# Optimization experiments

Hardware: AMD Instinct MI355X
Metric: run time of the kernel (lower is better)

## Reference

```python
import jax, jax.numpy as jnp
import numpy as np
import math

ALPHA = 0.25
GAMMA = 2.0
IMG = 640.0


def setup_inputs() -> dict:
    key = jax.random.key(0)
    k0, k1, k2, k3, k4, k5, k6, k7 = jax.random.split(key, 8)
    B, A, C, N = 8, 250000, 4, 16
    classifications = jax.random.uniform(k0, (B, A, C), minval=0.01, maxval=0.99, dtype=jnp.float32)
    regressions = jax.random.normal(k1, (B, A, 4), dtype=jnp.float32) * 0.1
    # anchors as (x1, y1, x2, y2) with x1<x2, y1<y2
    ctr = jax.random.uniform(k2, (A, 2), minval=0.0, maxval=IMG, dtype=jnp.float32)
    half = jax.random.uniform(k3, (A, 2), minval=2.0, maxval=32.0, dtype=jnp.float32)
    anchors_pos = jnp.concatenate([ctr - half, ctr + half], axis=1)
    # annotations: (cx, cy, angle, length, class); all valid (class != -1)
    ann_xy = jax.random.uniform(k4, (B, N, 2), minval=50.0, maxval=IMG - 50.0, dtype=jnp.float32)
    ann_th = jax.random.uniform(k5, (B, N, 1), minval=-math.pi / 2, maxval=math.pi / 2, dtype=jnp.float32)
    ann_len = jax.random.uniform(k6, (B, N, 1), minval=10.0, maxval=100.0, dtype=jnp.float32)
    ann_cls = jax.random.randint(k7, (B, N, 1), 0, C).astype(jnp.float32)
    annotations = jnp.concatenate([ann_xy, ann_th, ann_len, ann_cls], axis=2)
    return {"classifications": classifications, "regressions": regressions,
            "anchors_pos": anchors_pos, "annotations": annotations}


def coordinates_transform(anchors_pos):
    x1, y1, x2, y2 = anchors_pos[:, 0], anchors_pos[:, 1], anchors_pos[:, 2], anchors_pos[:, 3]
    ctr_x = (x1 + x2) / 2
    ctr_y = (y1 + y2) / 2
    width = x2 - x1
    height = y2 - y1
    length = jnp.sqrt((x2 - x1) ** 2 + (y2 - y1) ** 2)
    vert = x1 == x2
    safe_dx = jnp.where(vert, 1.0, x2 - x1)
    theta = jnp.where(vert, jnp.sign(y2 - y1) * (math.pi / 2), jnp.arctan((y2 - y1) / safe_dx))
    return ctr_x, ctr_y, width, height, length, theta


def calc_iou(anchors_pos, cal_annotations):
    # anchors_pos [A,4], cal_annotations [N,4] -> IoU [A,N]
    centers = cal_annotations[:, :2]
    ang = cal_annotations[:, 2]
    lng = cal_annotations[:, 3]
    dx = jnp.abs(0.5 * lng * jnp.cos(ang))[:, None]
    dy = jnp.abs(0.5 * lng * jnp.sin(ang))[:, None]
    lt = centers - jnp.concatenate([dx, dy], axis=1)
    rb = centers + jnp.concatenate([dx, dy], axis=1)
    bbox = jnp.concatenate([lt, rb], axis=1)  # [N,4]
    area = (bbox[:, 2] - bbox[:, 0]) * (bbox[:, 3] - bbox[:, 1])  # [N]
    iw = jnp.minimum(anchors_pos[:, 2][:, None], bbox[:, 2]) - jnp.maximum(anchors_pos[:, 0][:, None], bbox[:, 0])
    ih = jnp.minimum(anchors_pos[:, 3][:, None], bbox[:, 3]) - jnp.maximum(anchors_pos[:, 1][:, None], bbox[:, 1])
    iw = jnp.maximum(iw, 0.0)
    ih = jnp.maximum(ih, 0.0)
    a_area = ((anchors_pos[:, 2] - anchors_pos[:, 0]) * (anchors_pos[:, 3] - anchors_pos[:, 1]))[:, None]
    ua = jnp.maximum(a_area + area - iw * ih, 1e-8)
    return (iw * ih) / ua


def smooth_l1_rows(pred, gt):
    # per-row mean smooth-L1 over the 4 (cx, cy, theta, length) components
    d = pred - gt
    ad = jnp.abs(d)
    return jnp.mean(jnp.where(ad < 1.0, 0.5 * d * d, ad - 0.5), axis=-1)


def _per_image(classification, regression, annotation, anchors_pos, geom):
    A = anchors_pos.shape[0]
    C = classification.shape[1]
    cls = jnp.clip(classification, 1e-4, 1.0 - 1e-4)
    valid = annotation[:, 4] != -1.0  # [N]
    IoU = calc_iou(anchors_pos, annotation[:, :4])  # [A,N]
    IoU = jnp.where(valid[None, :], IoU, -1.0)
    IoU_max = IoU.max(axis=1)
    IoU_argmax = IoU.argmax(axis=1)
    pos = IoU_max >= 0.5
    neg = IoU_max < 0.4
    # targets: -1 ignore, 0 background, 1 assigned class
    targets = jnp.where((pos | neg)[:, None], 0.0, -1.0)  # [A,C]
    assigned = annotation[IoU_argmax]  # [A,5]
    onehot = jax.nn.one_hot(assigned[:, 4].astype(jnp.int32), C, dtype=jnp.float32)
    targets = jnp.where(pos[:, None] * onehot == 1.0, 1.0, targets)
    # force-assign best anchor for any annotation whose max IoU < 0.5
    ann_max = IoU.max(axis=0)     # [N]
    ann_arg = IoU.argmax(axis=0)  # [N]
    force = valid & (ann_max < 0.5)
    idx = jnp.where(force, ann_arg, A)  # A = out-of-bounds -> dropped
    ann_cls_idx = annotation[:, 4].astype(jnp.int32)
    targets = targets.at[idx].set(0.0, mode='drop')
    targets = targets.at[idx, ann_cls_idx].set(1.0, mode='drop')
    assigned = assigned.at[idx].set(annotation, mode='drop')
    positive = targets.sum(axis=-1) > 0.0  # [A]
    num_pos = positive.sum().astype(jnp.float32)
    # focal loss
    bce = -(targets * jnp.log(cls) + (1.0 - targets) * jnp.log(1.0 - cls))
    p_t = jnp.where(targets == 1.0, cls, 1.0 - cls)
    fl = (1.0 - p_t) ** GAMMA * bce
    alpha_f = jnp.where(targets == 1.0, ALPHA, 1.0 - ALPHA)
    fl = jnp.where(targets != -1.0, alpha_f * fl, 0.0)
    cls_loss = fl.sum() / jnp.maximum(num_pos, 1.0)
    ctr_x, ctr_y, w, h, L, th = geom
    pred_cx = regression[:, 0] * w + ctr_x
    pred_cy = regression[:, 1] * h + ctr_y
    pred_th = regression[:, 2] + th
    pred_len = jnp.exp(regression[:, 3]) * L
    pred_cal = jnp.stack([pred_cx, pred_cy, pred_th, pred_len], axis=1)  # [A,4]
    per_anchor = smooth_l1_rows(pred_cal, assigned[:, :4])
    reg_loss = jnp.sum(jnp.where(positive, per_anchor, 0.0)) / jnp.maximum(num_pos, 1.0)
    return cls_loss, reg_loss


def reference(classifications, regressions, anchors_pos, annotations):
    geom = coordinates_transform(anchors_pos)
    cls_l, reg_l = jax.vmap(lambda c, r, a: _per_image(c, r, a, anchors_pos, geom))(
        classifications, regressions, annotations)
    return (jnp.mean(cls_l, keepdims=True), jnp.mean(reg_l, keepdims=True))
```

## Files before the change

kernel.cpp:

```cpp
#include <hip/hip_runtime.h>
#include <math.h>

#define A_TOTAL 250000
#define BCNT 8
#define NANN 16
#define GX 128
#define NTHR 256
#define STRIDE (GX * NTHR)
#define IDXM 0x3FFFFu
#define QMASK 0xFFFC0000u


__device__ __forceinline__ float rfl(float x) {
    return __uint_as_float(__builtin_amdgcn_readfirstlane(__float_as_uint(x)));
}

__device__ __forceinline__ float4 pred_cal(float4 ap, float4 r, float aw, float ah) {
    float cxa = (ap.x + ap.z) * 0.5f, cya = (ap.y + ap.w) * 0.5f;
    float L = sqrtf(aw * aw + ah * ah);
    float th = (ap.x == ap.z) ? copysignf(1.5707963267948966f, ah) : atanf(ah / aw);
    return make_float4(r.x * aw + cxa, r.y * ah + cya, r.z + th, expf(r.w) * L);
}

__device__ __forceinline__ float sl1(float4 pr, float4 g) {
    float s = 0.f, d, ad;
    d = pr.x - g.x; ad = fabsf(d); s += (ad < 1.f) ? 0.5f * d * d : ad - 0.5f;
    d = pr.y - g.y; ad = fabsf(d); s += (ad < 1.f) ? 0.5f * d * d : ad - 0.5f;
    d = pr.z - g.z; ad = fabsf(d); s += (ad < 1.f) ? 0.5f * d * d : ad - 0.5f;
    d = pr.w - g.w; ad = fabsf(d); s += (ad < 1.f) ? 0.5f * d * d : ad - 0.5f;
    return s * 0.25f;
}

__device__ __forceinline__ float focal4m(float4 p4, unsigned mask) {
    float pv[4] = {p4.x, p4.y, p4.z, p4.w};
    float fl = 0.f;
#pragma unroll
    for (int c = 0; c < 4; c++) {
        float pc = fminf(fmaxf(pv[c], 1e-4f), 1.f - 1e-4f);
        fl += ((mask >> c) & 1) ? 0.25f * (1.f - pc) * (1.f - pc) * (-__logf(pc))
                                : 0.75f * pc * pc * (-__logf(1.f - pc));
    }
    return fl;
}

__global__ __launch_bounds__(256) void detloss_init(
    const float* __restrict__ ann, float* __restrict__ table)
{
    int tid = threadIdx.x;
    if (tid < BCNT * NANN) {
        int b = tid >> 4, n = tid & 15;
        const float* a5 = ann + tid * 5;
        float cx = a5[0], cy = a5[1], th = a5[2], ln = a5[3], cl = a5[4];
        bool valid = (cl != -1.0f);
        float dx = fabsf(0.5f * ln * cosf(th));
        float dy = fabsf(0.5f * ln * sinf(th));
        float x1 = cx - dx, y1 = cy - dy, x2 = cx + dx, y2 = cy + dy;
        float ar = (x2 - x1) * (y2 - y1);
        if (!valid) { x1 = y1 = x2 = y2 = 3.0e8f; ar = 1.0e30f; }
        float* tb = table + b * 160;
        tb[4 * n + 0] = x1; tb[4 * n + 1] = y1; tb[4 * n + 2] = x2; tb[4 * n + 3] = y2;
        tb[64 + n] = ar;
        tb[80 + 4 * n + 0] = cx; tb[80 + 4 * n + 1] = cy;
        tb[80 + 4 * n + 2] = th; tb[80 + 4 * n + 3] = ln;
        tb[144 + n] = cl;
    }
}

__global__ __launch_bounds__(NTHR, 4) void detloss_main(
    const float* __restrict__ cls, const float* __restrict__ reg,
    const float* __restrict__ anchors, const float* __restrict__ table,
    unsigned* __restrict__ part)
{
    int b = blockIdx.y;
    int tid = threadIdx.x;
    __shared__ float sGT[NANN][5];
    __shared__ unsigned sKey[4][NANN];
    __shared__ float sPart[4][3];

    const float* tb = table + b * 160;
    if (tid < NANN) {
        sGT[tid][0] = tb[80 + 4 * tid + 0]; sGT[tid][1] = tb[80 + 4 * tid + 1];
        sGT[tid][2] = tb[80 + 4 * tid + 2]; sGT[tid][3] = tb[80 + 4 * tid + 3];
        sGT[tid][4] = tb[144 + tid];
    }

    float sx1[NANN], sy1[NANN], sx2[NANN], sy2[NANN], bar[NANN];
#pragma unroll
    for (int n = 0; n < NANN; n++) {
        sx1[n] = rfl(tb[4 * n + 0]); sy1[n] = rfl(tb[4 * n + 1]);
        sx2[n] = rfl(tb[4 * n + 2]); sy2[n] = rfl(tb[4 * n + 3]);
        bar[n] = rfl(tb[64 + n]);
    }
    __syncthreads();

    unsigned bmk[NANN];
#pragma unroll
    for (int n = 0; n < NANN; n++) bmk[n] = 0u;
    float clsS = 0.f, regS = 0.f, nposS = 0.f;

    const float4* clsB = (const float4*)(cls + (size_t)b * A_TOTAL * 4);
    const float4* regB = (const float4*)(reg + (size_t)b * A_TOTAL * 4);
    const float4* anc4 = (const float4*)anchors;

    int a = blockIdx.x * NTHR + tid;
    float4 ap = anc4[a];
    while (a < A_TOTAL) {
        float4 p4 = clsB[a];
        int a2 = a + STRIDE;
        int apre = (a2 < A_TOTAL) ? a2 : a;
        float4 apn = anc4[apre];
        unsigned inv_a = IDXM - (unsigned)a;

        float aw = ap.z - ap.x, ah = ap.w - ap.y;
        float aarea = aw * ah;
        float best = 0.f; int barg = 0;
#pragma unroll
        for (int n = 0; n < NANN; n++) {
            float iw = fminf(ap.z, sx2[n]) - fmaxf(ap.x, sx1[n]);
            float ih = fminf(ap.w, sy2[n]) - fmaxf(ap.y, sy1[n]);
            iw = fmaxf(iw, 0.f); ih = fmaxf(ih, 0.f);
            float inter = iw * ih;
            float ua = fmaxf(aarea + bar[n] - inter, 1e-8f);
            float iou = inter * __builtin_amdgcn_rcpf(ua);
            if (iou > best) { best = iou; barg = n; }
            unsigned kc = (__float_as_uint(iou) & QMASK) | inv_a;
            bmk[n] = (kc > bmk[n]) ? kc : bmk[n];
        }
        if (best < 0.4f || best >= 0.5f) {
            bool pos = (best >= 0.5f);
            float pc0 = fminf(fmaxf(p4.x, 1e-4f), 1.f - 1e-4f);
            float pc1 = fminf(fmaxf(p4.y, 1e-4f), 1.f - 1e-4f);
            float pc2 = fminf(fmaxf(p4.z, 1e-4f), 1.f - 1e-4f);
            float pc3 = fminf(fmaxf(p4.w, 1e-4f), 1.f - 1e-4f);
            float fl = 0.75f * pc0 * pc0 * (-__logf(1.f - pc0))
                     + 0.75f * pc1 * pc1 * (-__logf(1.f - pc1))
                     + 0.75f * pc2 * pc2 * (-__logf(1.f - pc2))
                     + 0.75f * pc3 * pc3 * (-__logf(1.f - pc3));
            if (pos) {
                int ac = (int)sGT[barg][4];
                float pc = ac == 0 ? pc0 : ac == 1 ? pc1 : ac == 2 ? pc2 : pc3;
                fl += 0.25f * (1.f - pc) * (1.f - pc) * (-__logf(pc))
                    - 0.75f * pc * pc * (-__logf(1.f - pc));
                nposS += 1.f;
                float4 r = regB[a];
                float4 pr = pred_cal(ap, r, aw, ah);
                float4 g = make_float4(sGT[barg][0], sGT[barg][1], sGT[barg][2], sGT[barg][3]);
                regS += sl1(pr, g);
            }
            clsS += fl;
        }
        ap = apn; a = a2;
    }

    int lane = tid & 63, wv = tid >> 6;
#pragma unroll
    for (int n = 0; n < NANN; n++) {
        unsigned k = bmk[n];
#pragma unroll
        for (int off = 1; off < 64; off <<= 1) {
            unsigned o = __shfl_xor(k, off, 64);
            k = (o > k) ? o : k;
        }
        if (lane == 0) sKey[wv][n] = k;
    }
#pragma unroll
    for (int off = 1; off < 64; off <<= 1) {
        clsS  += __shfl_xor(clsS, off, 64);
        regS  += __shfl_xor(regS, off, 64);
        nposS += __shfl_xor(nposS, off, 64);
    }
    if (lane == 0) { sPart[wv][0] = clsS; sPart[wv][1] = regS; sPart[wv][2] = nposS; }
    __syncthreads();

    unsigned* pb = part + ((size_t)(b * GX + blockIdx.x)) * 32;
    if (tid < NANN) {
        unsigned m = sKey[0][tid];
#pragma unroll
        for (int w = 1; w < 4; w++) m = (sKey[w][tid] > m) ? sKey[w][tid] : m;
        pb[tid] = m;
    }
    if (tid == 0) {
        float c0 = 0, c1 = 0, c2 = 0;
        for (int w = 0; w < 4; w++) { c0 += sPart[w][0]; c1 += sPart[w][1]; c2 += sPart[w][2]; }
        ((float*)pb)[16] = c0;
        ((float*)pb)[17] = c1;
        ((float*)pb)[18] = c2;
    }
}

__global__ __launch_bounds__(256) void detloss_reduce(
    const float* __restrict__ cls, const float* __restrict__ reg,
    const float* __restrict__ anchors, const float* __restrict__ table,
    const unsigned* __restrict__ part, float* __restrict__ out)
{
    int tid = threadIdx.x;
    __shared__ unsigned rKey[BCNT][NANN];
    __shared__ float rAcc[BCNT][3];
    __shared__ int fForce[BCNT * NANN];
    __shared__ float fAcc[BCNT * 3];

    if (tid < BCNT * NANN) {
        int b = tid >> 4, n = tid & 15;
        unsigned m = 0u;
        for (int k = 0; k < GX; k++) {
            unsigned v = part[((size_t)(b * GX + k)) * 32 + n];
            m = (v > m) ? v : m;
        }
        rKey[b][n] = m;
    } else if (tid < BCNT * NANN + BCNT * 3) {
        int t = tid - BCNT * NANN; int b = t / 3, j = t % 3;
        float s = 0.f;
        for (int k = 0; k < GX; k++)
            s += ((const float*)part)[((size_t)(b * GX + k)) * 32 + 16 + j];
        rAcc[b][j] = s;
    }
    if (tid < BCNT * 3) fAcc[tid] = 0.f;
    __syncthreads();

    if (tid < BCNT * NANN) {
        int b = tid >> 4, n = tid & 15;
        unsigned k = rKey[b][n];
        float amax = __uint_as_float(k & QMASK);
        float cl = table[b * 160 + 144 + n];
        bool force = (cl != -1.f) && (amax < 0.5f);
        int anchor = (int)(IDXM - (k & IDXM));
        fForce[tid] = (force && anchor >= 0 && anchor < A_TOTAL) ? anchor : -1;
    }
    __syncthreads();

    if (tid < BCNT * NANN) {
        int fb = tid >> 4, fn = tid & 15;
        const float* tbf = table + fb * 160;
        int idx = fForce[tid];
        bool first = (idx >= 0);
        for (int m = 0; m < fn; m++) if (fForce[fb * NANN + m] == idx) first = false;
        if (idx >= 0 && first) {
            const float4* clsBf = (const float4*)(cls + (size_t)fb * A_TOTAL * 4);
            const float4* regBf = (const float4*)(reg + (size_t)fb * A_TOTAL * 4);
            float4 ap2 = ((const float4*)anchors)[idx];
            float aw = ap2.z - ap2.x, ah = ap2.w - ap2.y;
            float aarea = aw * ah;
            float best = 0.f; int barg = 0;
#pragma unroll
            for (int m = 0; m < NANN; m++) {
                float iw = fminf(ap2.z, tbf[4 * m + 2]) - fmaxf(ap2.x, tbf[4 * m + 0]);
                float ih = fminf(ap2.w, tbf[4 * m + 3]) - fmaxf(ap2.y, tbf[4 * m + 1]);
                iw = fmaxf(iw, 0.f); ih = fmaxf(ih, 0.f);
                float inter = iw * ih;
                float ua = fmaxf(aarea + tbf[64 + m] - inter, 1e-8f);
                float iou = inter * __builtin_amdgcn_rcpf(ua);
                if (iou > best) { best = iou; barg = m; }
            }
            float4 p4 = clsBf[idx];
            float oldc = 0.f, oldr = 0.f, oldn = 0.f;
            if (best < 0.4f || best >= 0.5f) {
                bool pos = (best >= 0.5f);
                unsigned msk = pos ? (1u << (int)tbf[144 + barg]) : 0u;
                oldc = focal4m(p4, msk);
                if (pos) {
                    oldn = 1.f;
                    float4 r = regBf[idx];
                    float4 pr = pred_cal(ap2, r, aw, ah);
                    float4 g = make_float4(tbf[80 + 4 * barg + 0], tbf[80 + 4 * barg + 1],
                                           tbf[80 + 4 * barg + 2], tbf[80 + 4 * barg + 3]);
                    oldr = sl1(pr, g);
                }
            }
            unsigned cmask = 0; int lastm = fn;
            for (int m = 0; m < NANN; m++)
                if (fForce[fb * NANN + m] == idx) { cmask |= 1u << (int)tbf[144 + m]; lastm = m; }
            float newc = focal4m(p4, cmask);
            float4 r = regBf[idx];
            float4 pr = pred_cal(ap2, r, aw, ah);
            float4 g = make_float4(tbf[80 + 4 * lastm + 0], tbf[80 + 4 * lastm + 1],
                                   tbf[80 + 4 * lastm + 2], tbf[80 + 4 * lastm + 3]);
            float newr = sl1(pr, g);
            atomicAdd(&fAcc[fb * 3 + 0], newc - oldc);
            atomicAdd(&fAcc[fb * 3 + 1], newr - oldr);
            atomicAdd(&fAcc[fb * 3 + 2], 1.f - oldn);
        }
    }
    __syncthreads();
    if (tid == 0) {
        float cm = 0.f, rm = 0.f;
        for (int b = 0; b < BCNT; b++) {
            float np = fmaxf(rAcc[b][2] + fAcc[b * 3 + 2], 1.f);
            cm += (rAcc[b][0] + fAcc[b * 3 + 0]) / np;
            rm += (rAcc[b][1] + fAcc[b * 3 + 1]) / np;
        }
        out[0] = cm * 0.125f;
        out[1] = rm * 0.125f;
    }
}

extern "C" void kernel_launch(void* const* d_in, const int* in_sizes, int n_in,
                              void* d_out, int out_size, void* d_ws, size_t ws_size,
                              hipStream_t stream) {
    const float* classifications = (const float*)d_in[0];
    const float* regressions     = (const float*)d_in[1];
    const float* anchors_pos     = (const float*)d_in[2];
    const float* annotations     = (const float*)d_in[3];
    float* out = (float*)d_out;

    char* ws = (char*)d_ws;
    float* table = (float*)(ws + 0);
    unsigned* part = (unsigned*)(ws + 8192);

    detloss_init<<<1, 256, 0, stream>>>(annotations, table);
    detloss_main<<<dim3(GX, BCNT), NTHR, 0, stream>>>(
        classifications, regressions, anchors_pos, table, part);
    detloss_reduce<<<1, 256, 0, stream>>>(
        classifications, regressions, anchors_pos, table, part, out);
}
```

Before: 51.30 us.

## Fold annotation table setup into main and reduce kernels, defer argmax recompute

Removes the separate init kernel launch: each main block now computes its annotation box bounds and areas inline from the raw annotations, and the reduce kernel builds its own shared-memory table. The hot IoU loop tracks only the max IoU with fmaxf, and the argmax index is recomputed by a second IoU pass only for positive anchors. This saves one launch and a dependent kernel boundary plus some per-anchor select instructions. In exchange every block redundantly evaluates sin/cos for 16 annotations, and positive anchors pay a second IoU loop.

```diff
diff --git a/kernel.cpp b/kernel.cpp
--- a/kernel.cpp
+++ b/kernel.cpp
@@ -43,32 +43,21 @@
     return fl;
 }
 
-__global__ __launch_bounds__(256) void detloss_init(
-    const float* __restrict__ ann, float* __restrict__ table)
+__device__ __forceinline__ void ann_consts(const float* a5,
+    float& x1, float& y1, float& x2, float& y2, float& ar)
 {
-    int tid = threadIdx.x;
-    if (tid < BCNT * NANN) {
-        int b = tid >> 4, n = tid & 15;
-        const float* a5 = ann + tid * 5;
-        float cx = a5[0], cy = a5[1], th = a5[2], ln = a5[3], cl = a5[4];
-        bool valid = (cl != -1.0f);
-        float dx = fabsf(0.5f * ln * cosf(th));
-        float dy = fabsf(0.5f * ln * sinf(th));
-        float x1 = cx - dx, y1 = cy - dy, x2 = cx + dx, y2 = cy + dy;
-        float ar = (x2 - x1) * (y2 - y1);
-        if (!valid) { x1 = y1 = x2 = y2 = 3.0e8f; ar = 1.0e30f; }
-        float* tb = table + b * 160;
-        tb[4 * n + 0] = x1; tb[4 * n + 1] = y1; tb[4 * n + 2] = x2; tb[4 * n + 3] = y2;
-        tb[64 + n] = ar;
-        tb[80 + 4 * n + 0] = cx; tb[80 + 4 * n + 1] = cy;
-        tb[80 + 4 * n + 2] = th; tb[80 + 4 * n + 3] = ln;
-        tb[144 + n] = cl;
-    }
+    float cx = a5[0], cy = a5[1], th = a5[2], ln = a5[3], cl = a5[4];
+    bool valid = (cl != -1.0f);
+    float dx = fabsf(0.5f * ln * cosf(th));
+    float dy = fabsf(0.5f * ln * sinf(th));
+    x1 = cx - dx; y1 = cy - dy; x2 = cx + dx; y2 = cy + dy;
+    ar = (x2 - x1) * (y2 - y1);
+    if (!valid) { x1 = y1 = x2 = y2 = 3.0e8f; ar = 1.0e30f; }
 }
 
 __global__ __launch_bounds__(NTHR, 4) void detloss_main(
     const float* __restrict__ cls, const float* __restrict__ reg,
-    const float* __restrict__ anchors, const float* __restrict__ table,
+    const float* __restrict__ anchors, const float* __restrict__ ann,
     unsigned* __restrict__ part)
 {
     int b = blockIdx.y;
@@ -77,19 +66,20 @@
     __shared__ unsigned sKey[4][NANN];
     __shared__ float sPart[4][3];
 
-    const float* tb = table + b * 160;
     if (tid < NANN) {
-        sGT[tid][0] = tb[80 + 4 * tid + 0]; sGT[tid][1] = tb[80 + 4 * tid + 1];
-        sGT[tid][2] = tb[80 + 4 * tid + 2]; sGT[tid][3] = tb[80 + 4 * tid + 3];
-        sGT[tid][4] = tb[144 + tid];
+        const float* a5 = ann + (b * NANN + tid) * 5;
+        sGT[tid][0] = a5[0]; sGT[tid][1] = a5[1]; sGT[tid][2] = a5[2];
+        sGT[tid][3] = a5[3]; sGT[tid][4] = a5[4];
     }
 
     float sx1[NANN], sy1[NANN], sx2[NANN], sy2[NANN], bar[NANN];
 #pragma unroll
     for (int n = 0; n < NANN; n++) {
-        sx1[n] = rfl(tb[4 * n + 0]); sy1[n] = rfl(tb[4 * n + 1]);
-        sx2[n] = rfl(tb[4 * n + 2]); sy2[n] = rfl(tb[4 * n + 3]);
-        bar[n] = rfl(tb[64 + n]);
+        const float* a5 = ann + (b * NANN + n) * 5;
+        float x1, y1, x2, y2, ar;
+        ann_consts(a5, x1, y1, x2, y2, ar);
+        sx1[n] = rfl(x1); sy1[n] = rfl(y1); sx2[n] = rfl(x2); sy2[n] = rfl(y2);
+        bar[n] = rfl(ar);
     }
     __syncthreads();
 
@@ -113,7 +103,7 @@
 
         float aw = ap.z - ap.x, ah = ap.w - ap.y;
         float aarea = aw * ah;
-        float best = 0.f; int barg = 0;
+        float best = 0.f;
 #pragma unroll
         for (int n = 0; n < NANN; n++) {
             float iw = fminf(ap.z, sx2[n]) - fmaxf(ap.x, sx1[n]);
@@ -122,7 +112,7 @@
             float inter = iw * ih;
             float ua = fmaxf(aarea + bar[n] - inter, 1e-8f);
             float iou = inter * __builtin_amdgcn_rcpf(ua);
-            if (iou > best) { best = iou; barg = n; }
+            best = fmaxf(best, iou);
             unsigned kc = (__float_as_uint(iou) & QMASK) | inv_a;
             bmk[n] = (kc > bmk[n]) ? kc : bmk[n];
         }
@@ -137,6 +127,17 @@
                      + 0.75f * pc2 * pc2 * (-__logf(1.f - pc2))
                      + 0.75f * pc3 * pc3 * (-__logf(1.f - pc3));
             if (pos) {
+                int barg = 0;
+#pragma unroll
+                for (int n = NANN - 1; n >= 0; n--) {
+                    float iw = fminf(ap.z, sx2[n]) - fmaxf(ap.x, sx1[n]);
+                    float ih = fminf(ap.w, sy2[n]) - fmaxf(ap.y, sy1[n]);
+                    iw = fmaxf(iw, 0.f); ih = fmaxf(ih, 0.f);
+                    float inter = iw * ih;
+                    float ua = fmaxf(aarea + bar[n] - inter, 1e-8f);
+                    float iou = inter * __builtin_amdgcn_rcpf(ua);
+                    if (iou == best) barg = n;
+                }
                 int ac = (int)sGT[barg][4];
                 float pc = ac == 0 ? pc0 : ac == 1 ? pc1 : ac == 2 ? pc2 : pc3;
                 fl += 0.25f * (1.f - pc) * (1.f - pc) * (-__logf(pc))
@@ -190,14 +191,25 @@
 
 __global__ __launch_bounds__(256) void detloss_reduce(
     const float* __restrict__ cls, const float* __restrict__ reg,
-    const float* __restrict__ anchors, const float* __restrict__ table,
+    const float* __restrict__ anchors, const float* __restrict__ ann,
     const unsigned* __restrict__ part, float* __restrict__ out)
 {
     int tid = threadIdx.x;
+    __shared__ float fTab[BCNT * NANN][10];
     __shared__ unsigned rKey[BCNT][NANN];
     __shared__ float rAcc[BCNT][3];
     __shared__ int fForce[BCNT * NANN];
     __shared__ float fAcc[BCNT * 3];
+
+    if (tid < BCNT * NANN) {
+        const float* a5 = ann + tid * 5;
+        float x1, y1, x2, y2, ar;
+        ann_consts(a5, x1, y1, x2, y2, ar);
+        fTab[tid][0] = x1; fTab[tid][1] = y1; fTab[tid][2] = x2; fTab[tid][3] = y2;
+        fTab[tid][4] = ar;
+        fTab[tid][5] = a5[0]; fTab[tid][6] = a5[1]; fTab[tid][7] = a5[2];
+        fTab[tid][8] = a5[3]; fTab[tid][9] = a5[4];
+    }
 
     if (tid < BCNT * NANN) {
         int b = tid >> 4, n = tid & 15;
@@ -221,7 +233,7 @@
         int b = tid >> 4, n = tid & 15;
         unsigned k = rKey[b][n];
         float amax = __uint_as_float(k & QMASK);
-        float cl = table[b * 160 + 144 + n];
+        float cl = fTab[b * NANN + n][9];
         bool force = (cl != -1.f) && (amax < 0.5f);
         int anchor = (int)(IDXM - (k & IDXM));
         fForce[tid] = (force && anchor >= 0 && anchor < A_TOTAL) ? anchor : -1;
@@ -230,7 +242,6 @@
 
     if (tid < BCNT * NANN) {
         int fb = tid >> 4, fn = tid & 15;
-        const float* tbf = table + fb * 160;
         int idx = fForce[tid];
         bool first = (idx >= 0);
         for (int m = 0; m < fn; m++) if (fForce[fb * NANN + m] == idx) first = false;
@@ -240,41 +251,54 @@
             float4 ap2 = ((const float4*)anchors)[idx];
             float aw = ap2.z - ap2.x, ah = ap2.w - ap2.y;
             float aarea = aw * ah;
-            float best = 0.f; int barg = 0;
+            float best = 0.f;
 #pragma unroll
             for (int m = 0; m < NANN; m++) {
-                float iw = fminf(ap2.z, tbf[4 * m + 2]) - fmaxf(ap2.x, tbf[4 * m + 0]);
-                float ih = fminf(ap2.w, tbf[4 * m + 3]) - fmaxf(ap2.y, tbf[4 * m + 1]);
+                const float* t = fTab[fb * NANN + m];
+                float iw = fminf(ap2.z, t[2]) - fmaxf(ap2.x, t[0]);
+                float ih = fminf(ap2.w, t[3]) - fmaxf(ap2.y, t[1]);
                 iw = fmaxf(iw, 0.f); ih = fmaxf(ih, 0.f);
                 float inter = iw * ih;
-                float ua = fmaxf(aarea + tbf[64 + m] - inter, 1e-8f);
+                float ua = fmaxf(aarea + t[4] - inter, 1e-8f);
                 float iou = inter * __builtin_amdgcn_rcpf(ua);
-                if (iou > best) { best = iou; barg = m; }
+                best = fmaxf(best, iou);
+            }
+            int barg = 0;
+#pragma unroll
+            for (int m = NANN - 1; m >= 0; m--) {
+                const float* t = fTab[fb * NANN + m];
+                float iw = fminf(ap2.z, t[2]) - fmaxf(ap2.x, t[0]);
+                float ih = fminf(ap2.w, t[3]) - fmaxf(ap2.y, t[1]);
+                iw = fmaxf(iw, 0.f); ih = fmaxf(ih, 0.f);
+                float inter = iw * ih;
+                float ua = fmaxf(aarea + t[4] - inter, 1e-8f);
+                float iou = inter * __builtin_amdgcn_rcpf(ua);
+                if (iou == best) barg = m;
             }
             float4 p4 = clsBf[idx];
             float oldc = 0.f, oldr = 0.f, oldn = 0.f;
             if (best < 0.4f || best >= 0.5f) {
                 bool pos = (best >= 0.5f);
-                unsigned msk = pos ? (1u << (int)tbf[144 + barg]) : 0u;
+                unsigned msk = pos ? (1u << (int)fTab[fb * NANN + barg][9]) : 0u;
                 oldc = focal4m(p4, msk);
                 if (pos) {
                     oldn = 1.f;
                     float4 r = regBf[idx];
                     float4 pr = pred_cal(ap2, r, aw, ah);
-                    float4 g = make_float4(tbf[80 + 4 * barg + 0], tbf[80 + 4 * barg + 1],
-                                           tbf[80 + 4 * barg + 2], tbf[80 + 4 * barg + 3]);
-                    oldr = sl1(pr, g);
+                    const float* t = fTab[fb * NANN + barg];
+                    oldr = sl1(pr, make_float4(t[5], t[6], t[7], t[8]));
                 }
             }
             unsigned cmask = 0; int lastm = fn;
             for (int m = 0; m < NANN; m++)
-                if (fForce[fb * NANN + m] == idx) { cmask |= 1u << (int)tbf[144 + m]; lastm = m; }
+                if (fForce[fb * NANN + m] == idx) {
+                    cmask |= 1u << (int)fTab[fb * NANN + m][9]; lastm = m;
+                }
             float newc = focal4m(p4, cmask);
             float4 r = regBf[idx];
             float4 pr = pred_cal(ap2, r, aw, ah);
-            float4 g = make_float4(tbf[80 + 4 * lastm + 0], tbf[80 + 4 * lastm + 1],
-                                   tbf[80 + 4 * lastm + 2], tbf[80 + 4 * lastm + 3]);
-            float newr = sl1(pr, g);
+            const float* t = fTab[fb * NANN + lastm];
+            float newr = sl1(pr, make_float4(t[5], t[6], t[7], t[8]));
             atomicAdd(&fAcc[fb * 3 + 0], newc - oldc);
             atomicAdd(&fAcc[fb * 3 + 1], newr - oldr);
             atomicAdd(&fAcc[fb * 3 + 2], 1.f - oldn);
@@ -302,13 +326,10 @@
     const float* annotations     = (const float*)d_in[3];
     float* out = (float*)d_out;
 
-    char* ws = (char*)d_ws;
-    float* table = (float*)(ws + 0);
-    unsigned* part = (unsigned*)(ws + 8192);
-
-    detloss_init<<<1, 256, 0, stream>>>(annotations, table);
+    unsigned* part = (unsigned*)d_ws;
+
     detloss_main<<<dim3(GX, BCNT), NTHR, 0, stream>>>(
-        classifications, regressions, anchors_pos, table, part);
+        classifications, regressions, anchors_pos, annotations, part);
     detloss_reduce<<<1, 256, 0, stream>>>(
-        classifications, regressions, anchors_pos, table, part, out);
-}
+        classifications, regressions, anchors_pos, annotations, part, out);
+}
```

Measured after the change: 52.29 us. No clear change (+1.9%).
